# Performance work log

Hardware: AMD Instinct MI355X
Metric: run time of the kernel (lower is better)

The kernel has to match this reference:

```python
import jax, jax.numpy as jnp
import numpy as np

N_NODES = 10000
N_EDGES = 160000
HIDDEN = 64
NUM_RBF = 32
Q_DIM = 8
CUTOFF_UPPER = 5.0


def silu(x):
    return x * jax.nn.sigmoid(x)


def tensor_norm(X):
    # X: [n, 3, 3, H] -> [n, H] (Frobenius norm squared over the 3x3 dims)
    return (X * X).sum(axis=(1, 2))


def decompose_tensor(X):
    # X: [n, 3, 3, H] -> I: [n, H] (trace/3), A: antisym [n,3,3,H], S: sym traceless [n,3,3,H]
    eye = jnp.eye(3, dtype=X.dtype)[None, :, :, None]
    I = jnp.einsum('naah->nh', X) / 3.0
    Xt = X.transpose(0, 2, 1, 3)
    A = 0.5 * (X - Xt)
    S = 0.5 * (X + Xt) - I[:, None, None, :] * eye
    return I, A, S


def compose_tensor(I, A, S):
    eye = jnp.eye(3, dtype=A.dtype)[None, :, :, None]
    return I[:, None, None, :] * eye + A + S


def tmm(P, Q):
    # 3x3 matmul per (atom, channel): [n,3,3,H] x [n,3,3,H] -> [n,3,3,H]
    return jnp.einsum('nach,ncbh->nabh', P, Q)


def setup_inputs() -> dict:
    key = jax.random.key(0)
    ks = jax.random.split(key, 16)
    H = HIDDEN
    inp = {
        'X': jax.random.normal(ks[0], (N_NODES, 3, 3, H), jnp.float32),
        'charges': jax.random.normal(ks[1], (N_NODES, Q_DIM), jnp.float32),
        'edge_weight': jax.random.uniform(ks[2], (N_EDGES,), jnp.float32) * CUTOFF_UPPER,
        'edge_attr': jax.random.normal(ks[3], (N_EDGES, NUM_RBF), jnp.float32),
        'edge_index': jax.random.randint(ks[4], (2, N_EDGES), 0, N_NODES, jnp.int32),
    }
    d_in = NUM_RBF + 2 * Q_DIM
    inp['Ws1'] = jax.random.normal(ks[5], (d_in, H), jnp.float32) / np.sqrt(d_in).astype(np.float32)
    inp['bs1'] = jnp.zeros((H,), jnp.float32)
    inp['Ws2'] = jax.random.normal(ks[6], (H, 2 * H), jnp.float32) / np.sqrt(H).astype(np.float32)
    inp['bs2'] = jnp.zeros((2 * H,), jnp.float32)
    inp['Ws3'] = jax.random.normal(ks[7], (2 * H, 3 * H), jnp.float32) / np.sqrt(2 * H).astype(np.float32)
    inp['bs3'] = jnp.zeros((3 * H,), jnp.float32)
    for i in range(6):
        inp['Wt%d' % i] = jax.random.normal(ks[8 + i], (H, H), jnp.float32) / np.sqrt(H).astype(np.float32)
    return inp


def reference(X, charges, edge_weight, edge_attr, Ws1, bs1, Ws2, bs2, Ws3, bs3,
              Wt0, Wt1, Wt2, Wt3, Wt4, Wt5, edge_index):
    H = HIDDEN
    n = X.shape[0]
    row, col = edge_index[0], edge_index[1]
    # cosine cutoff (cutoff_lower = 0)
    C = 0.5 * (jnp.cos(edge_weight * (jnp.pi / CUTOFF_UPPER)) + 1.0)
    C = C * (edge_weight < CUTOFF_UPPER).astype(X.dtype)
    # edge scalar MLP on [rbf, q_i, q_j]
    h = jnp.concatenate([edge_attr, charges[row], charges[col]], axis=-1)
    h = silu(h @ Ws1 + bs1)
    h = silu(h @ Ws2 + bs2)
    h = silu(h @ Ws3 + bs3)
    w = (h * C[:, None]).reshape(h.shape[0], 3, H)  # [E, 3, H]
    # normalize node tensors
    X = X / (tensor_norm(X) + 1.0)[:, None, None, :]
    I, A, S = decompose_tensor(X)
    I = I @ Wt0
    A = A @ Wt1
    S = S @ Wt2
    Y = compose_tensor(I, A, S)
    # message passing: gather I/A/S at source (edge_index[1]), weight per component, scatter-add at dest (edge_index[0])
    eye = jnp.eye(3, dtype=X.dtype)[None, :, :, None]
    msg_e = ((w[:, 0] * I[col])[:, None, None, :] * eye
             + w[:, 1][:, None, None, :] * A[col]
             + w[:, 2][:, None, None, :] * S[col])  # [E, 3, 3, H]
    msg = jax.ops.segment_sum(msg_e, row, num_segments=n)  # [n, 3, 3, H]
    # O(3): C = msg @ Y + Y @ msg (3x3 matmul per channel)
    Cm = tmm(msg, Y) + tmm(Y, msg)
    I2, A2, S2 = decompose_tensor(Cm)
    normp1 = tensor_norm(Cm) + 1.0
    I2 = I2 / normp1
    A2 = A2 / normp1[:, None, None, :]
    S2 = S2 / normp1[:, None, None, :]
    I2 = I2 @ Wt3
    A2 = A2 @ Wt4
    S2 = S2 @ Wt5
    dX = compose_tensor(I2, A2, S2)
    return X + dX + tmm(dX, dX)
```

## Files before the change

### kernel.cpp

```cpp
#include <hip/hip_runtime.h>
#include <math.h>

#define HD 64

typedef _Float16 half8 __attribute__((ext_vector_type(8)));
typedef float floatx4 __attribute__((ext_vector_type(4)));

__device__ __forceinline__ float silu_f(float x) {
    return x * __builtin_amdgcn_rcpf(1.0f + __expf(-x));
}

__global__ __launch_bounds__(256) void node_pre(
    const float* __restrict__ X,
    const float* __restrict__ Wt0, const float* __restrict__ Wt1, const float* __restrict__ Wt2,
    float* __restrict__ Tn, _Float16* __restrict__ TnH, int N)
{
    int sub = threadIdx.x >> 6;
    int h = threadIdx.x & 63;
    int n = blockIdx.x * 4 + sub;
    int nn = (n < N) ? n : (N - 1);

    const float* Xb = X + (size_t)nn * 9 * HD + h;
    float x[9];
    float nrm = 0.f;
#pragma unroll
    for (int i = 0; i < 9; ++i) { x[i] = Xb[i * HD]; nrm += x[i] * x[i]; }
    float inv = 1.0f / (nrm + 1.0f);
#pragma unroll
    for (int i = 0; i < 9; ++i) x[i] *= inv;

    float I0 = (x[0] + x[4] + x[8]) * (1.0f / 3.0f);
    __shared__ float comp[4][10][HD];
    comp[sub][0][h] = I0;
    comp[sub][1][h] = 0.5f * (x[1] - x[3]);
    comp[sub][2][h] = 0.5f * (x[2] - x[6]);
    comp[sub][3][h] = 0.5f * (x[5] - x[7]);
    comp[sub][4][h] = x[0] - I0;
    comp[sub][5][h] = 0.5f * (x[1] + x[3]);
    comp[sub][6][h] = 0.5f * (x[2] + x[6]);
    comp[sub][7][h] = x[4] - I0;
    comp[sub][8][h] = 0.5f * (x[5] + x[7]);
    comp[sub][9][h] = x[8] - I0;
    __syncthreads();
    float acc[10];
#pragma unroll
    for (int i = 0; i < 10; ++i) acc[i] = 0.f;
    for (int k = 0; k < HD; ++k) {
        float w0 = Wt0[k * HD + h];
        float w1 = Wt1[k * HD + h];
        float w2 = Wt2[k * HD + h];
        acc[0] += comp[sub][0][k] * w0;
        acc[1] += comp[sub][1][k] * w1;
        acc[2] += comp[sub][2][k] * w1;
        acc[3] += comp[sub][3][k] * w1;
#pragma unroll
        for (int j = 0; j < 6; ++j) acc[4 + j] += comp[sub][4 + j][k] * w2;
    }
    if (n < N) {
        float* tp = Tn + (size_t)n * 640 + h;
        _Float16* th = TnH + (size_t)n * 640 + h;
#pragma unroll
        for (int i = 0; i < 10; ++i) {
            tp[i * 64] = acc[i];
            th[i * 64] = (_Float16)acc[i];
        }
    }
}

__global__ __launch_bounds__(256) void count_kernel(
    const int* __restrict__ edge_index, int* __restrict__ cnt, int E)
{
    int e = blockIdx.x * 256 + threadIdx.x;
    if (e < E) atomicAdd(&cnt[edge_index[e]], 1);
}

__global__ __launch_bounds__(1024) void scan_kernel(
    const int* __restrict__ cnt, int* __restrict__ offs, int* __restrict__ curs, int N)
{
    __shared__ int partials[16];
    __shared__ int base_s;
    int tid = threadIdx.x, wid = tid >> 6, lane = tid & 63;
    if (tid == 0) base_s = 0;
    __syncthreads();
    for (int start = 0; start < N; start += 1024) {
        int i = start + tid;
        int v = (i < N) ? cnt[i] : 0;
        int s = v;
#pragma unroll
        for (int d = 1; d < 64; d <<= 1) {
            int t = __shfl_up(s, d, 64);
            if (lane >= d) s += t;
        }
        if (lane == 63) partials[wid] = s;
        __syncthreads();
        if (tid == 0) {
            int run = base_s;
#pragma unroll
            for (int w = 0; w < 16; ++w) { int t = partials[w]; partials[w] = run; run += t; }
            base_s = run;
        }
        __syncthreads();
        int excl = partials[wid] + s - v;
        if (i < N) { offs[i] = excl; curs[i] = excl; }
        __syncthreads();
    }
    if (tid == 0) offs[N] = base_s;
}

__global__ __launch_bounds__(256) void place_kernel(
    const int* __restrict__ edge_index, int* __restrict__ curs,
    int* __restrict__ rank, int* __restrict__ colP, int E)
{
    int e = blockIdx.x * 256 + threadIdx.x;
    if (e < E) {
        int p = atomicAdd(&curs[edge_index[e]], 1);
        rank[e] = p;
        colP[p] = edge_index[E + e];
    }
}

__global__ __launch_bounds__(256) void wconv(
    const float* __restrict__ Ws1, const float* __restrict__ Ws2, const float* __restrict__ Ws3,
    _Float16* __restrict__ W1f, _Float16* __restrict__ W2f, _Float16* __restrict__ W3f)
{
    int id = blockIdx.x * 256 + threadIdx.x;
    if (id < 4096) {
        int i = id & 7, l = (id >> 3) & 63, t = id >> 9;
        int s = t >> 2, nt = t & 3;
        int k = s * 32 + (l >> 4) * 8 + i;
        int n = nt * 16 + (l & 15);
        W1f[id] = (k < 48) ? (_Float16)Ws1[k * 64 + n] : (_Float16)0.f;
    } else if (id < 4096 + 8192) {
        int j = id - 4096;
        int i = j & 7, l = (j >> 3) & 63, t = j >> 9;
        int s = t >> 3, nt = t & 7;
        int k = s * 32 + (l >> 4) * 8 + i;
        int n = nt * 16 + (l & 15);
        W2f[j] = (_Float16)Ws2[k * 128 + n];
    } else if (id < 4096 + 8192 + 24576) {
        int j = id - 4096 - 8192;
        int i = j & 7, l = (j >> 3) & 63, t = j >> 9;
        int s = t / 12, nt = t % 12;
        int k = s * 32 + (l >> 4) * 8 + i;
        int n = nt * 16 + (l & 15);
        W3f[j] = (_Float16)Ws3[k * 192 + n];
    }
}

__global__ __launch_bounds__(256, 4) void mlp_mfma(
    const float* __restrict__ edge_attr, const float* __restrict__ charges,
    const float* __restrict__ edge_weight, const int* __restrict__ edge_index,
    const int* __restrict__ rank,
    const _Float16* __restrict__ W1f, const float* __restrict__ bs1,
    const _Float16* __restrict__ W2f, const float* __restrict__ bs2,
    const _Float16* __restrict__ W3f, const float* __restrict__ bs3,
    _Float16* __restrict__ bufH, int E)
{
    __shared__ __align__(16) _Float16 ins[64][72];
    __shared__ __align__(16) _Float16 act[4][16][200];
    __shared__ int rankS[64];
    __shared__ float cvs[64];

    int tid = threadIdx.x;
    int base = blockIdx.x * 64;

    for (int idx = tid; idx < 1024; idx += 256) {
        int e_l = idx >> 4, f = idx & 15;
        int e = base + e_l;
        int ee = (e < E) ? e : (E - 1);
        float4 v = make_float4(0.f, 0.f, 0.f, 0.f);
        if (f < 8) {
            v = *(const float4*)(edge_attr + (size_t)ee * 32 + f * 4);
        } else if (f < 10) {
            int r = edge_index[ee];
            v = *(const float4*)(charges + (size_t)r * 8 + (f - 8) * 4);
        } else if (f < 12) {
            int c = edge_index[E + ee];
            v = *(const float4*)(charges + (size_t)c * 8 + (f - 10) * 4);
        }
        ins[e_l][f * 4 + 0] = (_Float16)v.x;
        ins[e_l][f * 4 + 1] = (_Float16)v.y;
        ins[e_l][f * 4 + 2] = (_Float16)v.z;
        ins[e_l][f * 4 + 3] = (_Float16)v.w;
    }
    if (tid < 64) {
        int e = base + tid;
        int ee = (e < E) ? e : (E - 1);
        rankS[tid] = rank[ee];
        float wgt = edge_weight[ee];
        float cv = 0.5f * (__cosf(wgt * 0.6283185307179586f) + 1.0f);
        cvs[tid] = (wgt < 5.0f) ? cv : 0.0f;
    }
    __syncthreads();

    int wv = tid >> 6, l = tid & 63;
    int row16 = l & 15, quad = l >> 4;

    half8 A[4];
    A[0] = *(const half8*)&ins[wv * 16 + row16][quad * 8];
    A[1] = *(const half8*)&ins[wv * 16 + row16][32 + quad * 8];
    floatx4 acc1[4];
#pragma unroll
    for (int nt = 0; nt < 4; ++nt) {
        floatx4 c = {0.f, 0.f, 0.f, 0.f};
        c = __builtin_amdgcn_mfma_f32_16x16x32_f16(
                A[0], *(const half8*)(W1f + ((size_t)(0 * 4 + nt) * 64 + l) * 8), c, 0, 0, 0);
        c = __builtin_amdgcn_mfma_f32_16x16x32_f16(
                A[1], *(const half8*)(W1f + ((size_t)(1 * 4 + nt) * 64 + l) * 8), c, 0, 0, 0);
        acc1[nt] = c;
    }
#pragma unroll
    for (int nt = 0; nt < 4; ++nt) {
        float b = bs1[nt * 16 + row16];
#pragma unroll
        for (int r = 0; r < 4; ++r)
            act[wv][quad * 4 + r][nt * 16 + row16] = (_Float16)silu_f(acc1[nt][r] + b);
    }

    A[0] = *(const half8*)&act[wv][row16][quad * 8];
    A[1] = *(const half8*)&act[wv][row16][32 + quad * 8];
    floatx4 acc2[8];
#pragma unroll
    for (int nt = 0; nt < 8; ++nt) {
        floatx4 c = {0.f, 0.f, 0.f, 0.f};
        c = __builtin_amdgcn_mfma_f32_16x16x32_f16(
                A[0], *(const half8*)(W2f + ((size_t)(0 * 8 + nt) * 64 + l) * 8), c, 0, 0, 0);
        c = __builtin_amdgcn_mfma_f32_16x16x32_f16(
                A[1], *(const half8*)(W2f + ((size_t)(1 * 8 + nt) * 64 + l) * 8), c, 0, 0, 0);
        acc2[nt] = c;
    }
#pragma unroll
    for (int nt = 0; nt < 8; ++nt) {
        float b = bs2[nt * 16 + row16];
#pragma unroll
        for (int r = 0; r < 4; ++r)
            act[wv][quad * 4 + r][nt * 16 + row16] = (_Float16)silu_f(acc2[nt][r] + b);
    }

    A[0] = *(const half8*)&act[wv][row16][quad * 8];
    A[1] = *(const half8*)&act[wv][row16][32 + quad * 8];
    A[2] = *(const half8*)&act[wv][row16][64 + quad * 8];
    A[3] = *(const half8*)&act[wv][row16][96 + quad * 8];

    float cvrow[4];
#pragma unroll
    for (int r = 0; r < 4; ++r) cvrow[r] = cvs[wv * 16 + quad * 4 + r];

    floatx4 acc3[12];
#pragma unroll
    for (int nt = 0; nt < 12; ++nt) {
        floatx4 c = {0.f, 0.f, 0.f, 0.f};
#pragma unroll
        for (int s = 0; s < 4; ++s)
            c = __builtin_amdgcn_mfma_f32_16x16x32_f16(
                    A[s], *(const half8*)(W3f + ((size_t)(s * 12 + nt) * 64 + l) * 8), c, 0, 0, 0);
        acc3[nt] = c;
    }
#pragma unroll
    for (int nt = 0; nt < 12; ++nt) {
        float b = bs3[nt * 16 + row16];
#pragma unroll
        for (int r = 0; r < 4; ++r)
            act[wv][quad * 4 + r][nt * 16 + row16] =
                (_Float16)(silu_f(acc3[nt][r] + b) * cvrow[r]);
    }
    {
        int fr = l >> 2;
        int ef = base + wv * 16 + fr;
        if (ef < E) {
            _Float16* dst = bufH + (size_t)rankS[wv * 16 + fr] * 192;
#pragma unroll
            for (int i = 0; i < 6; ++i) {
                int j = (l & 3) + i * 4;
                *(half8*)(dst + j * 8) = *(const half8*)&act[wv][fr][j * 8];
            }
        }
    }
}

__global__ __launch_bounds__(128) void msg_kernel(
    const _Float16* __restrict__ bufH, const int* __restrict__ colP,
    const int* __restrict__ offs, const _Float16* __restrict__ TnH,
    float* __restrict__ Mn, int N)
{
    int n = blockIdx.x * 2 + (threadIdx.x >> 6);
    if (n >= N) return;
    int lane = threadIdx.x & 63;
    int beg = offs[n], end = offs[n + 1];
    float a0 = 0.f, a1 = 0.f, a2 = 0.f, a3 = 0.f, a4 = 0.f;
    float a5 = 0.f, a6 = 0.f, a7 = 0.f, a8 = 0.f, a9 = 0.f;
#pragma unroll 4
    for (int idx = beg; idx < end; ++idx) {
        int c = colP[idx];
        const _Float16* wp = bufH + (size_t)idx * 192;
        float w0 = (float)wp[lane];
        float w1 = (float)wp[64 + lane];
        float w2 = (float)wp[128 + lane];
        const _Float16* tp = TnH + (size_t)c * 640;
        a0 += w0 * (float)tp[lane];
        a1 += w1 * (float)tp[64 + lane];
        a2 += w1 * (float)tp[128 + lane];
        a3 += w1 * (float)tp[192 + lane];
        a4 += w2 * (float)tp[256 + lane];
        a5 += w2 * (float)tp[320 + lane];
        a6 += w2 * (float)tp[384 + lane];
        a7 += w2 * (float)tp[448 + lane];
        a8 += w2 * (float)tp[512 + lane];
        a9 += w2 * (float)tp[576 + lane];
    }
    float* mp = Mn + (size_t)n * 640;
    mp[lane] = a0;
    mp[64 + lane] = a1;  mp[128 + lane] = a2; mp[192 + lane] = a3;
    mp[256 + lane] = a4; mp[320 + lane] = a5; mp[384 + lane] = a6;
    mp[448 + lane] = a7; mp[512 + lane] = a8; mp[576 + lane] = a9;
}

__global__ __launch_bounds__(256) void node_post(
    const float* __restrict__ X,
    const float* __restrict__ Tn, const float* __restrict__ Mn,
    const float* __restrict__ Wt3, const float* __restrict__ Wt4, const float* __restrict__ Wt5,
    float* __restrict__ out, int N)
{
    int sub = threadIdx.x >> 6;
    int h = threadIdx.x & 63;
    int n = blockIdx.x * 4 + sub;
    int nn = (n < N) ? n : (N - 1);

    const float* Xb = X + (size_t)nn * 9 * HD + h;
    float x[9];
    float nr = 0.f;
#pragma unroll
    for (int i = 0; i < 9; ++i) { x[i] = Xb[i * HD]; nr += x[i] * x[i]; }
    float xinv = 1.0f / (nr + 1.0f);
#pragma unroll
    for (int i = 0; i < 9; ++i) x[i] *= xinv;

    const float* tp = Tn + (size_t)nn * 640 + h;
    const float* mp = Mn + (size_t)nn * 640 + h;
    float yI = tp[0], mI = mp[0];
    float yA[3], yS[6], mA[3], mS[6];
#pragma unroll
    for (int j = 0; j < 3; ++j) { yA[j] = tp[(1 + j) * 64]; mA[j] = mp[(1 + j) * 64]; }
#pragma unroll
    for (int j = 0; j < 6; ++j) { yS[j] = tp[(4 + j) * 64]; mS[j] = mp[(4 + j) * 64]; }

    float M[3][3] = {
        { mI + mS[0],     mA[0] + mS[1],   mA[1] + mS[2] },
        { -mA[0] + mS[1], mI + mS[3],      mA[2] + mS[4] },
        { -mA[1] + mS[2], -mA[2] + mS[4],  mI + mS[5] } };
    float Y[3][3] = {
        { yI + yS[0],     yA[0] + yS[1],   yA[1] + yS[2] },
        { -yA[0] + yS[1], yI + yS[3],      yA[2] + yS[4] },
        { -yA[1] + yS[2], -yA[2] + yS[4],  yI + yS[5] } };

    float Cm[3][3];
    float nrm = 0.f;
#pragma unroll
    for (int a = 0; a < 3; ++a) {
#pragma unroll
        for (int b = 0; b < 3; ++b) {
            float s = 0.f;
#pragma unroll
            for (int c = 0; c < 3; ++c) s += M[a][c] * Y[c][b] + Y[a][c] * M[c][b];
            Cm[a][b] = s;
            nrm += s * s;
        }
    }
    float inv = 1.0f / (nrm + 1.0f);
    float tr3 = (Cm[0][0] + Cm[1][1] + Cm[2][2]) * (1.0f / 3.0f);

    __shared__ float comp[4][10][HD];
    comp[sub][0][h] = tr3 * inv;
    comp[sub][1][h] = 0.5f * (Cm[0][1] - Cm[1][0]) * inv;
    comp[sub][2][h] = 0.5f * (Cm[0][2] - Cm[2][0]) * inv;
    comp[sub][3][h] = 0.5f * (Cm[1][2] - Cm[2][1]) * inv;
    comp[sub][4][h] = (Cm[0][0] - tr3) * inv;
    comp[sub][5][h] = 0.5f * (Cm[0][1] + Cm[1][0]) * inv;
    comp[sub][6][h] = 0.5f * (Cm[0][2] + Cm[2][0]) * inv;
    comp[sub][7][h] = (Cm[1][1] - tr3) * inv;
    comp[sub][8][h] = 0.5f * (Cm[1][2] + Cm[2][1]) * inv;
    comp[sub][9][h] = (Cm[2][2] - tr3) * inv;
    __syncthreads();

    float acc[10];
#pragma unroll
    for (int i = 0; i < 10; ++i) acc[i] = 0.f;
    for (int k = 0; k < HD; ++k) {
        float w3 = Wt3[k * HD + h];
        float w4 = Wt4[k * HD + h];
        float w5 = Wt5[k * HD + h];
        acc[0] += comp[sub][0][k] * w3;
        acc[1] += comp[sub][1][k] * w4;
        acc[2] += comp[sub][2][k] * w4;
        acc[3] += comp[sub][3][k] * w4;
#pragma unroll
        for (int j = 0; j < 6; ++j) acc[4 + j] += comp[sub][4 + j][k] * w5;
    }
    float D[3][3] = {
        { acc[0] + acc[4],  acc[1] + acc[5],  acc[2] + acc[6] },
        { -acc[1] + acc[5], acc[0] + acc[7],  acc[3] + acc[8] },
        { -acc[2] + acc[6], -acc[3] + acc[8], acc[0] + acc[9] } };

    if (n < N) {
        float* ob = out + (size_t)n * 9 * HD + h;
#pragma unroll
        for (int a = 0; a < 3; ++a) {
#pragma unroll
            for (int b = 0; b < 3; ++b) {
                float s = 0.f;
#pragma unroll
                for (int c = 0; c < 3; ++c) s += D[a][c] * D[c][b];
                ob[(a * 3 + b) * HD] = x[a * 3 + b] + D[a][b] + s;
            }
        }
    }
}

extern "C" void kernel_launch(void* const* d_in, const int* in_sizes, int n_in,
                              void* d_out, int out_size, void* d_ws, size_t ws_size,
                              hipStream_t stream)
{
    const float* X           = (const float*)d_in[0];
    const float* charges     = (const float*)d_in[1];
    const float* edge_weight = (const float*)d_in[2];
    const float* edge_attr   = (const float*)d_in[3];
    const int*   edge_index  = (const int*)d_in[4];
    const float* Ws1 = (const float*)d_in[5];
    const float* bs1 = (const float*)d_in[6];
    const float* Ws2 = (const float*)d_in[7];
    const float* bs2 = (const float*)d_in[8];
    const float* Ws3 = (const float*)d_in[9];
    const float* bs3 = (const float*)d_in[10];
    const float* Wt0 = (const float*)d_in[11];
    const float* Wt1 = (const float*)d_in[12];
    const float* Wt2 = (const float*)d_in[13];
    const float* Wt3 = (const float*)d_in[14];
    const float* Wt4 = (const float*)d_in[15];
    const float* Wt5 = (const float*)d_in[16];

    int N = in_sizes[0] / (9 * HD);
    int E = in_sizes[2];

    float* ws = (float*)d_ws;
    float* Tn  = ws;
    float* Mn  = Tn + (size_t)N * 640;
    _Float16* TnH  = (_Float16*)(Mn + (size_t)N * 640);
    _Float16* bufH = TnH + (size_t)N * 640;
    int* cnt   = (int*)(bufH + (size_t)E * 192);
    int* offs  = cnt + N;
    int* curs  = offs + N + 1;
    int* rank  = curs + N;
    int* colP  = rank + E;
    size_t fofs = ((size_t)((char*)(colP + E) - (char*)d_ws) + 15) & ~(size_t)15;
    _Float16* W1f = (_Float16*)((char*)d_ws + fofs);
    _Float16* W2f = W1f + 4096;
    _Float16* W3f = W2f + 8192;

    hipMemsetAsync(cnt, 0, (size_t)N * sizeof(int), stream);

    int nbE256 = (E + 255) / 256;
    count_kernel<<<nbE256, 256, 0, stream>>>(edge_index, cnt, E);
    scan_kernel<<<1, 1024, 0, stream>>>(cnt, offs, curs, N);
    place_kernel<<<nbE256, 256, 0, stream>>>(edge_index, curs, rank, colP, E);

    wconv<<<144, 256, 0, stream>>>(Ws1, Ws2, Ws3, W1f, W2f, W3f);

    node_pre<<<(N + 3) / 4, 256, 0, stream>>>(X, Wt0, Wt1, Wt2, Tn, TnH, N);

    int nbE64 = (E + 63) / 64;
    mlp_mfma<<<nbE64, 256, 0, stream>>>(edge_attr, charges, edge_weight, edge_index,
                                        rank, W1f, bs1, W2f, bs2, W3f, bs3, bufH, E);

    msg_kernel<<<(N + 1) / 2, 128, 0, stream>>>(bufH, colP, offs, TnH, Mn, N);

    node_post<<<(N + 3) / 4, 256, 0, stream>>>(X, Tn, Mn, Wt3, Wt4, Wt5, (float*)d_out, N);
}
```

Before: 186.7 us.

## Make MLP kernel wave-private without block sync; split message gather across two waves

The edge MLP kernel now has each wave stage its own 16 edges' inputs in its private slice of the shared activation buffer, which removes the separate input buffer and the block-wide barrier. It also raises the occupancy hint from 4 to 6 blocks. The message kernel now uses two waves per node, one for the I and A components and one for the S components. This doubles parallelism and cuts per-thread accumulators, at the cost of reading the edge list and column indices twice.

```diff
diff --git a/kernel.cpp b/kernel.cpp
--- a/kernel.cpp
+++ b/kernel.cpp
@@ -4,6 +4,7 @@
 #define HD 64
 
 typedef _Float16 half8 __attribute__((ext_vector_type(8)));
+typedef _Float16 half4v __attribute__((ext_vector_type(4)));
 typedef float floatx4 __attribute__((ext_vector_type(4)));
 
 __device__ __forceinline__ float silu_f(float x) {
@@ -147,7 +148,7 @@
     }
 }
 
-__global__ __launch_bounds__(256, 4) void mlp_mfma(
+__global__ __launch_bounds__(256, 6) void mlp_mfma(
     const float* __restrict__ edge_attr, const float* __restrict__ charges,
     const float* __restrict__ edge_weight, const int* __restrict__ edge_index,
     const int* __restrict__ rank,
@@ -156,16 +157,19 @@
     const _Float16* __restrict__ W3f, const float* __restrict__ bs3,
     _Float16* __restrict__ bufH, int E)
 {
-    __shared__ __align__(16) _Float16 ins[64][72];
-    __shared__ __align__(16) _Float16 act[4][16][200];
-    __shared__ int rankS[64];
-    __shared__ float cvs[64];
+    __shared__ __align__(16) _Float16 act[4][16][208];
+    __shared__ float cvsS[4][16];
+    __shared__ int rankSS[4][16];
 
     int tid = threadIdx.x;
-    int base = blockIdx.x * 64;
-
-    for (int idx = tid; idx < 1024; idx += 256) {
-        int e_l = idx >> 4, f = idx & 15;
+    int wv = tid >> 6, l = tid & 63;
+    int base = blockIdx.x * 64 + wv * 16;
+    int row16 = l & 15, quad = l >> 4;
+
+#pragma unroll
+    for (int i = 0; i < 4; ++i) {
+        int slot = l + i * 64;
+        int e_l = slot >> 4, f = slot & 15;
         int e = base + e_l;
         int ee = (e < E) ? e : (E - 1);
         float4 v = make_float4(0.f, 0.f, 0.f, 0.f);
@@ -178,27 +182,21 @@
             int c = edge_index[E + ee];
             v = *(const float4*)(charges + (size_t)c * 8 + (f - 10) * 4);
         }
-        ins[e_l][f * 4 + 0] = (_Float16)v.x;
-        ins[e_l][f * 4 + 1] = (_Float16)v.y;
-        ins[e_l][f * 4 + 2] = (_Float16)v.z;
-        ins[e_l][f * 4 + 3] = (_Float16)v.w;
-    }
-    if (tid < 64) {
-        int e = base + tid;
+        half4v hv = { (_Float16)v.x, (_Float16)v.y, (_Float16)v.z, (_Float16)v.w };
+        *(half4v*)&act[wv][e_l][f * 4] = hv;
+    }
+    if (l < 16) {
+        int e = base + l;
         int ee = (e < E) ? e : (E - 1);
-        rankS[tid] = rank[ee];
+        rankSS[wv][l] = rank[ee];
         float wgt = edge_weight[ee];
         float cv = 0.5f * (__cosf(wgt * 0.6283185307179586f) + 1.0f);
-        cvs[tid] = (wgt < 5.0f) ? cv : 0.0f;
-    }
-    __syncthreads();
-
-    int wv = tid >> 6, l = tid & 63;
-    int row16 = l & 15, quad = l >> 4;
+        cvsS[wv][l] = (wgt < 5.0f) ? cv : 0.0f;
+    }
 
     half8 A[4];
-    A[0] = *(const half8*)&ins[wv * 16 + row16][quad * 8];
-    A[1] = *(const half8*)&ins[wv * 16 + row16][32 + quad * 8];
+    A[0] = *(const half8*)&act[wv][row16][quad * 8];
+    A[1] = *(const half8*)&act[wv][row16][32 + quad * 8];
     floatx4 acc1[4];
 #pragma unroll
     for (int nt = 0; nt < 4; ++nt) {
@@ -214,11 +212,11 @@
         float b = bs1[nt * 16 + row16];
 #pragma unroll
         for (int r = 0; r < 4; ++r)
-            act[wv][quad * 4 + r][nt * 16 + row16] = (_Float16)silu_f(acc1[nt][r] + b);
-    }
-
-    A[0] = *(const half8*)&act[wv][row16][quad * 8];
-    A[1] = *(const half8*)&act[wv][row16][32 + quad * 8];
+            act[wv][quad * 4 + r][64 + nt * 16 + row16] = (_Float16)silu_f(acc1[nt][r] + b);
+    }
+
+    A[0] = *(const half8*)&act[wv][row16][64 + quad * 8];
+    A[1] = *(const half8*)&act[wv][row16][96 + quad * 8];
     floatx4 acc2[8];
 #pragma unroll
     for (int nt = 0; nt < 8; ++nt) {
@@ -244,7 +242,7 @@
 
     float cvrow[4];
 #pragma unroll
-    for (int r = 0; r < 4; ++r) cvrow[r] = cvs[wv * 16 + quad * 4 + r];
+    for (int r = 0; r < 4; ++r) cvrow[r] = cvsS[wv][quad * 4 + r];
 
     floatx4 acc3[12];
 #pragma unroll
@@ -266,9 +264,9 @@
     }
     {
         int fr = l >> 2;
-        int ef = base + wv * 16 + fr;
+        int ef = base + fr;
         if (ef < E) {
-            _Float16* dst = bufH + (size_t)rankS[wv * 16 + fr] * 192;
+            _Float16* dst = bufH + (size_t)rankSS[wv][fr] * 192;
 #pragma unroll
             for (int i = 0; i < 6; ++i) {
                 int j = (l & 3) + i * 4;
@@ -278,41 +276,53 @@
     }
 }
 
-__global__ __launch_bounds__(128) void msg_kernel(
+__global__ __launch_bounds__(256) void msg_kernel(
     const _Float16* __restrict__ bufH, const int* __restrict__ colP,
     const int* __restrict__ offs, const _Float16* __restrict__ TnH,
     float* __restrict__ Mn, int N)
 {
-    int n = blockIdx.x * 2 + (threadIdx.x >> 6);
+    int n = blockIdx.x * 2 + (threadIdx.x >> 7);
     if (n >= N) return;
+    int half = (threadIdx.x >> 6) & 1;
     int lane = threadIdx.x & 63;
     int beg = offs[n], end = offs[n + 1];
-    float a0 = 0.f, a1 = 0.f, a2 = 0.f, a3 = 0.f, a4 = 0.f;
-    float a5 = 0.f, a6 = 0.f, a7 = 0.f, a8 = 0.f, a9 = 0.f;
+
+    if (half == 0) {
+        float a0 = 0.f, a1 = 0.f, a2 = 0.f, a3 = 0.f;
 #pragma unroll 4
-    for (int idx = beg; idx < end; ++idx) {
-        int c = colP[idx];
-        const _Float16* wp = bufH + (size_t)idx * 192;
-        float w0 = (float)wp[lane];
-        float w1 = (float)wp[64 + lane];
-        float w2 = (float)wp[128 + lane];
-        const _Float16* tp = TnH + (size_t)c * 640;
-        a0 += w0 * (float)tp[lane];
-        a1 += w1 * (float)tp[64 + lane];
-        a2 += w1 * (float)tp[128 + lane];
-        a3 += w1 * (float)tp[192 + lane];
-        a4 += w2 * (float)tp[256 + lane];
-        a5 += w2 * (float)tp[320 + lane];
-        a6 += w2 * (float)tp[384 + lane];
-        a7 += w2 * (float)tp[448 + lane];
-        a8 += w2 * (float)tp[512 + lane];
-        a9 += w2 * (float)tp[576 + lane];
-    }
-    float* mp = Mn + (size_t)n * 640;
-    mp[lane] = a0;
-    mp[64 + lane] = a1;  mp[128 + lane] = a2; mp[192 + lane] = a3;
-    mp[256 + lane] = a4; mp[320 + lane] = a5; mp[384 + lane] = a6;
-    mp[448 + lane] = a7; mp[512 + lane] = a8; mp[576 + lane] = a9;
+        for (int idx = beg; idx < end; ++idx) {
+            int c = colP[idx];
+            const _Float16* wp = bufH + (size_t)idx * 192;
+            float w0 = (float)wp[lane];
+            float w1 = (float)wp[64 + lane];
+            const _Float16* tp = TnH + (size_t)c * 640;
+            a0 += w0 * (float)tp[lane];
+            a1 += w1 * (float)tp[64 + lane];
+            a2 += w1 * (float)tp[128 + lane];
+            a3 += w1 * (float)tp[192 + lane];
+        }
+        float* mp = Mn + (size_t)n * 640;
+        mp[lane] = a0;
+        mp[64 + lane] = a1; mp[128 + lane] = a2; mp[192 + lane] = a3;
+    } else {
+        float a4 = 0.f, a5 = 0.f, a6 = 0.f, a7 = 0.f, a8 = 0.f, a9 = 0.f;
+#pragma unroll 4
+        for (int idx = beg; idx < end; ++idx) {
+            int c = colP[idx];
+            const _Float16* wp = bufH + (size_t)idx * 192;
+            float w2 = (float)wp[128 + lane];
+            const _Float16* tp = TnH + (size_t)c * 640;
+            a4 += w2 * (float)tp[256 + lane];
+            a5 += w2 * (float)tp[320 + lane];
+            a6 += w2 * (float)tp[384 + lane];
+            a7 += w2 * (float)tp[448 + lane];
+            a8 += w2 * (float)tp[512 + lane];
+            a9 += w2 * (float)tp[576 + lane];
+        }
+        float* mp = Mn + (size_t)n * 640;
+        mp[256 + lane] = a4; mp[320 + lane] = a5; mp[384 + lane] = a6;
+        mp[448 + lane] = a7; mp[512 + lane] = a8; mp[576 + lane] = a9;
+    }
 }
 
 __global__ __launch_bounds__(256) void node_post(
@@ -471,7 +481,7 @@
     mlp_mfma<<<nbE64, 256, 0, stream>>>(edge_attr, charges, edge_weight, edge_index,
                                         rank, W1f, bs1, W2f, bs2, W3f, bs3, bufH, E);
 
-    msg_kernel<<<(N + 1) / 2, 128, 0, stream>>>(bufH, colP, offs, TnH, Mn, N);
+    msg_kernel<<<(N + 1) / 2, 256, 0, stream>>>(bufH, colP, offs, TnH, Mn, N);
 
     node_post<<<(N + 3) / 4, 256, 0, stream>>>(X, Tn, Mn, Wt3, Wt4, Wt5, (float*)d_out, N);
 }
```

Result: no change. 184.3 us (-1.3%).
